# Kernel tuning notes

Hardware: AMD Instinct MI355X
Metric: run time of the kernel (lower is better)

The kernel has to match this reference:

```python
import jax, jax.numpy as jnp
import numpy as np

K = 3; STRIDE = 1; PAD = 1; DIL = 1; DG = 1  # deformable_groups = 1


def _conv2d(x, w, b, stride, pad):
    out = jax.lax.conv_general_dilated(
        x, w, (stride, stride), [(pad, pad), (pad, pad)],
        dimension_numbers=("NCHW", "OIHW", "NCHW"))
    return out + b[None, :, None, None]


def setup_inputs() -> dict:
    key = jax.random.key(0)
    k1, k2, k3 = jax.random.split(key, 3)
    B, Cin, H, W = 4, 64, 160, 160
    Cout = 64
    inp = {
        "input": jax.random.normal(k1, (B, Cin, H, W), dtype=jnp.float32),
        # offset/mask conv: dg*3*k*k = 27 output channels; scaled small so offsets are O(few px)
        "w_off": jax.random.normal(k2, (DG * 3 * K * K, Cin, K, K), dtype=jnp.float32) * 0.1,
        "b_off": jnp.zeros((DG * 3 * K * K,), dtype=jnp.float32),
        "w_dcn": jax.random.normal(k3, (Cout, Cin, K, K), dtype=jnp.float32) * 0.05,
        "b_dcn": jnp.zeros((Cout,), dtype=jnp.float32),
    }
    return inp


def _dcnv2(x, offset, mask, w, b):
    # x: [B,C,H,W]; offset: [B,2*kk,Ho,Wo]; mask: [B,kk,Ho,Wo] (already sigmoided)
    B, C, H, W = x.shape
    kk = K * K
    Ho, Wo = offset.shape[2], offset.shape[3]
    # mmcv channel layout within a deformable group: channel 2*p = y-offset, 2*p+1 = x-offset
    off = offset.reshape(B, kk, 2, Ho, Wo)
    off_y, off_x = off[:, :, 0], off[:, :, 1]            # [B,kk,Ho,Wo]

    ki, kj = jnp.meshgrid(jnp.arange(K), jnp.arange(K), indexing="ij")
    ki = ki.reshape(kk).astype(jnp.float32)
    kj = kj.reshape(kk).astype(jnp.float32)
    hs = (jnp.arange(Ho) * STRIDE - PAD).astype(jnp.float32)
    ws = (jnp.arange(Wo) * STRIDE - PAD).astype(jnp.float32)
    base_y = hs[None, :, None] + (ki * DIL)[:, None, None]   # [kk,Ho,1]
    base_x = ws[None, None, :] + (kj * DIL)[:, None, None]   # [kk,1,Wo]

    y = base_y[None] + off_y   # [B,kk,Ho,Wo]
    xx = base_x[None] + off_x

    y0 = jnp.floor(y); x0 = jnp.floor(xx)
    dy = y - y0; dx = xx - x0
    y0i = y0.astype(jnp.int32); y1i = y0i + 1
    x0i = x0.astype(jnp.int32); x1i = x0i + 1

    def gather(img, yi, xi):
        # img [C,H,W]; yi/xi [kk,Ho,Wo]; zero padding outside the image
        valid = (yi >= 0) & (yi < H) & (xi >= 0) & (xi < W)
        yc = jnp.clip(yi, 0, H - 1)
        xc = jnp.clip(xi, 0, W - 1)
        return img[:, yc, xc] * valid[None]   # [C,kk,Ho,Wo]

    gb = jax.vmap(gather)
    g00 = gb(x, y0i, x0i)
    g01 = gb(x, y0i, x1i)
    g10 = gb(x, y1i, x0i)
    g11 = gb(x, y1i, x1i)

    w00 = ((1 - dy) * (1 - dx))[:, None]   # [B,1,kk,Ho,Wo]
    w01 = ((1 - dy) * dx)[:, None]
    w10 = (dy * (1 - dx))[:, None]
    w11 = (dy * dx)[:, None]
    val = g00 * w00 + g01 * w01 + g10 * w10 + g11 * w11   # [B,C,kk,Ho,Wo]

    val = val * mask[:, None]                              # modulation
    Cout = w.shape[0]
    out = jnp.einsum("bckhw,ock->bohw", val, w.reshape(Cout, C, kk))
    return out + b[None, :, None, None]


def reference(input, w_off, b_off, w_dcn, b_dcn):
    om = _conv2d(input, w_off, b_off, STRIDE, PAD)   # [B, 3*kk, Ho, Wo]
    o1, o2, mask = jnp.split(om, 3, axis=1)
    offset = jnp.concatenate([o1, o2], axis=1)
    mask = jax.nn.sigmoid(mask)
    return _dcnv2(input, offset, mask, w_dcn, b_dcn)
```

## Files before the change

### kernel.cpp

```cpp
#include <hip/hip_runtime.h>
#include <math.h>

#define B_   4
#define CIN  64
#define H_   160
#define W_   160
#define COUT 64
#define OFFC 27
#define HW_  (H_ * W_)
#define NPIX (B_ * HW_)

#define TILE_P 64
#define VP2    65


__global__ __launch_bounds__(256) void k_transpose_nhwc(const float* __restrict__ in,
                                                        float* __restrict__ out) {
    __shared__ float tile[CIN][33];
    int blk = blockIdx.x;
    int wc  = blk % 5;
    int by  = blk / 5;
    int y   = by % H_;
    int b   = by / H_;
    int w0  = wc * 32;
    int t   = threadIdx.x;

    int wi = t & 31, ch = t >> 5;
#pragma unroll
    for (int r = 0; r < 8; ++r) {
        int c = r * 8 + ch;
        tile[c][wi] = in[((b * CIN + c) * H_ + y) * W_ + w0 + wi];
    }
    __syncthreads();
    int c2 = t & 63, wj = t >> 6;
#pragma unroll
    for (int r = 0; r < 8; ++r) {
        int wi2 = r * 4 + wj;
        out[((b * H_ + y) * W_ + w0 + wi2) * CIN + c2] = tile[c2][wi2];
    }
}

__global__ void k_transpose_w(const float* __restrict__ w, float* __restrict__ wT) {
    int i  = blockIdx.x * 256 + threadIdx.x;
    int co = i & 63;
    int kc = i >> 6;
    int c  = kc & 63;
    int k  = kc >> 6;
    wT[i] = w[(co * CIN + c) * 9 + k];
}

__global__ __launch_bounds__(256, 4) void k_offconv(const float* __restrict__ in,
                                                    const float* __restrict__ wo,
                                                    const float* __restrict__ bo,
                                                    float* __restrict__ om2) {
    int bid = (int)blockIdx.x;
    int id  = (bid & 7) * 150 + (bid >> 3);
    int g   = id % 3;
    int pb  = id / 3;
    int p   = pb * 256 + threadIdx.x;
    int b   = p / HW_;
    int rem = p - b * HW_;
    int y   = rem / W_;
    int x   = rem - y * W_;

    int   off[9];
    float valid[9];
#pragma unroll
    for (int di = 0; di < 3; ++di) {
        int yy = y + di - 1;
        int yc = min(max(yy, 0), H_ - 1);
        bool yok = (yy >= 0) & (yy < H_);
#pragma unroll
        for (int dj = 0; dj < 3; ++dj) {
            int xx = x + dj - 1;
            int xc = min(max(xx, 0), W_ - 1);
            bool ok = yok & (xx >= 0) & (xx < W_);
            off[di * 3 + dj]   = yc * W_ + xc;
            valid[di * 3 + dj] = ok ? 1.f : 0.f;
        }
    }

    float acc[9];
#pragma unroll
    for (int j = 0; j < 9; ++j) acc[j] = bo[g * 9 + j];

    const float* inb = in + (size_t)b * CIN * HW_;
    const float* wg  = wo + (size_t)(g * 9) * 576;
    for (int c = 0; c < CIN; c += 2) {
        float va[9], vb[9];
#pragma unroll
        for (int tp = 0; tp < 9; ++tp)
            va[tp] = inb[c * HW_ + off[tp]] * valid[tp];
#pragma unroll
        for (int tp = 0; tp < 9; ++tp)
            vb[tp] = inb[(c + 1) * HW_ + off[tp]] * valid[tp];
#pragma unroll
        for (int j = 0; j < 9; ++j) {
#pragma unroll
            for (int tp = 0; tp < 9; ++tp)
                acc[j] += va[tp] * wg[j * 576 + c * 9 + tp];
#pragma unroll
            for (int tp = 0; tp < 9; ++tp)
                acc[j] += vb[tp] * wg[j * 576 + (c + 1) * 9 + tp];
        }
    }
#pragma unroll
    for (int j = 0; j < 9; ++j)
        om2[(size_t)(g * 9 + j) * NPIX + p] = acc[j];
}

template <bool NHWC>
__global__ __launch_bounds__(256, 6) void k_dcn(const float* __restrict__ xsrc,
                                                const float* __restrict__ om2,
                                                const float* __restrict__ wT,
                                                const float* __restrict__ bd,
                                                float* __restrict__ out) {
    __shared__ __align__(16) float sk[TILE_P * 8];
    __shared__ __align__(16) float vals[64 * VP2];

    int t   = threadIdx.x;
    int bid = (int)blockIdx.x;
    int blk = (bid & 7) * ((NPIX / TILE_P) / 8) + (bid >> 3);
    int p0  = blk * TILE_P;
    int b   = p0 / HW_;
    int rb  = p0 - b * HW_;

    int lane = t & 63;
    int co0  = __builtin_amdgcn_readfirstlane((t >> 6) << 4);

    float acc[16];
#pragma unroll
    for (int j = 0; j < 16; ++j) acc[j] = bd[co0 + j];

    const float* base = xsrc + (size_t)b * CIN * HW_;

    for (int k = 0; k < 9; ++k) {
        __syncthreads();

        if (t < TILE_P) {
            int p   = p0 + t;
            int rem = rb + t;
            int y   = rem / W_;
            int x   = rem - y * W_;
            float oy = om2[(size_t)(2 * k) * NPIX + p];
            float ox = om2[(size_t)(2 * k + 1) * NPIX + p];
            float mr = om2[(size_t)(18 + k) * NPIX + p];
            float m  = 1.f / (1.f + expf(-mr));
            int ki = k / 3, kj = k - ki * 3;
            float fy  = (float)(y - 1 + ki) + oy;
            float fx  = (float)(x - 1 + kj) + ox;
            float fy0 = floorf(fy), fx0 = floorf(fx);
            float dy = fy - fy0, dx = fx - fx0;
            int iy = (int)fy0, ix = (int)fx0;
            bool yok0 = (iy >= 0) & (iy < H_);
            bool yok1 = (iy + 1 >= 0) & (iy + 1 < H_);
            bool xok0 = (ix >= 0) & (ix < W_);
            bool xok1 = (ix + 1 >= 0) & (ix + 1 < W_);
            int iyc0 = min(max(iy, 0), H_ - 1);
            int iyc1 = min(max(iy + 1, 0), H_ - 1);
            int ixc0 = min(max(ix, 0), W_ - 1);
            int ixc1 = min(max(ix + 1, 0), W_ - 1);
            const int mul = NHWC ? 64 : 1;
            float4 swt, sof;
            swt.x = (1.f - dy) * (1.f - dx) * m * (float)(yok0 & xok0);
            swt.y = (1.f - dy) * dx         * m * (float)(yok0 & xok1);
            swt.z = dy * (1.f - dx)         * m * (float)(yok1 & xok0);
            swt.w = dy * dx                 * m * (float)(yok1 & xok1);
            sof.x = __int_as_float((iyc0 * W_ + ixc0) * mul);
            sof.y = __int_as_float((iyc0 * W_ + ixc1) * mul);
            sof.z = __int_as_float((iyc1 * W_ + ixc0) * mul);
            sof.w = __int_as_float((iyc1 * W_ + ixc1) * mul);
            *reinterpret_cast<float4*>(sk + t * 8)     = swt;
            *reinterpret_cast<float4*>(sk + t * 8 + 4) = sof;
        }
        __syncthreads();

        {
            int c     = lane;
            int cterm = NHWC ? c : c * HW_;
#pragma unroll 4
            for (int it = 0; it < 16; ++it) {
                int pix = (t >> 6) + 4 * it;
                const float* s = sk + pix * 8;
                float4 sw = *reinterpret_cast<const float4*>(s);
                float4 so = *reinterpret_cast<const float4*>(s + 4);
                float g00 = base[__float_as_int(so.x) + cterm];
                float g01 = base[__float_as_int(so.y) + cterm];
                float g10 = base[__float_as_int(so.z) + cterm];
                float g11 = base[__float_as_int(so.w) + cterm];
                vals[c * VP2 + pix] = g00 * sw.x + g01 * sw.y + g10 * sw.z + g11 * sw.w;
            }
        }
        __syncthreads();

        const float* wk = wT + (k * 64) * 64 + co0;
#pragma unroll 4
        for (int c = 0; c < 64; ++c) {
            float v = vals[c * VP2 + lane];
            const float* wp = wk + c * 64;
            float4 wv0 = *reinterpret_cast<const float4*>(wp);
            float4 wv1 = *reinterpret_cast<const float4*>(wp + 4);
            float4 wv2 = *reinterpret_cast<const float4*>(wp + 8);
            float4 wv3 = *reinterpret_cast<const float4*>(wp + 12);
            acc[0]  += v * wv0.x;  acc[1]  += v * wv0.y;
            acc[2]  += v * wv0.z;  acc[3]  += v * wv0.w;
            acc[4]  += v * wv1.x;  acc[5]  += v * wv1.y;
            acc[6]  += v * wv1.z;  acc[7]  += v * wv1.w;
            acc[8]  += v * wv2.x;  acc[9]  += v * wv2.y;
            acc[10] += v * wv2.z;  acc[11] += v * wv2.w;
            acc[12] += v * wv3.x;  acc[13] += v * wv3.y;
            acc[14] += v * wv3.z;  acc[15] += v * wv3.w;
        }
    }

    __syncthreads();
#pragma unroll
    for (int j = 0; j < 16; ++j)
        vals[(co0 + j) * VP2 + lane] = acc[j];
    __syncthreads();
#pragma unroll 4
    for (int it = 0; it < 16; ++it) {
        int i  = t + it * 256;
        int co = i >> 6;
        int px = i & 63;
        out[((size_t)(b * COUT + co)) * HW_ + rb + px] = vals[co * VP2 + px];
    }
}

extern "C" void kernel_launch(void* const* d_in, const int* in_sizes, int n_in,
                              void* d_out, int out_size, void* d_ws, size_t ws_size,
                              hipStream_t stream) {
    const float* input = (const float*)d_in[0];
    const float* w_off = (const float*)d_in[1];
    const float* b_off = (const float*)d_in[2];
    const float* w_dcn = (const float*)d_in[3];
    const float* b_dcn = (const float*)d_in[4];
    float* out = (float*)d_out;

    const size_t XN_F = (size_t)NPIX * CIN;
    const size_t OM_F = (size_t)NPIX * OFFC;
    const size_t WT_F = 576 * 64;
    const size_t need_full = (XN_F + OM_F + WT_F) * sizeof(float);

    float* ws = (float*)d_ws;
    if (ws_size >= need_full) {
        float* x_nhwc = ws;
        float* om2    = ws + XN_F;
        float* wT     = om2 + OM_F;
        k_transpose_nhwc<<<dim3(B_ * H_ * 5), dim3(256), 0, stream>>>(input, x_nhwc);
        k_transpose_w<<<dim3(144), dim3(256), 0, stream>>>(w_dcn, wT);
        k_offconv<<<dim3(1200), dim3(256), 0, stream>>>(input, w_off, b_off, om2);
        k_dcn<true><<<dim3(NPIX / TILE_P), dim3(256), 0, stream>>>(x_nhwc, om2, wT, b_dcn, out);
    } else {
        float* om2 = ws;
        float* wT  = om2 + OM_F;
        k_transpose_w<<<dim3(144), dim3(256), 0, stream>>>(w_dcn, wT);
        k_offconv<<<dim3(1200), dim3(256), 0, stream>>>(input, w_off, b_off, om2);
        k_dcn<false><<<dim3(NPIX / TILE_P), dim3(256), 0, stream>>>(input, om2, wT, b_dcn, out);
    }
}
```

Before: 319.9 us.

## Precompute all tap sample weights and double-buffer gathered values in DCN kernel

The DCN kernel now computes bilinear weights and offsets for all 9 kernel taps up front using every thread, instead of 64 threads per tap. Gathered values are double-buffered in shared memory so the gather for tap k+1 overlaps the FMA accumulation for tap k, cutting the barriers per tap from three to one. This roughly doubles LDS use, so the occupancy hint drops from 6 to 3 blocks per CU. The offset conv loop is also changed from manual 2-channel unrolling to a pragma unroll 2.

```diff
diff --git a/kernel.cpp b/kernel.cpp
--- a/kernel.cpp
+++ b/kernel.cpp
@@ -86,22 +86,17 @@
 
     const float* inb = in + (size_t)b * CIN * HW_;
     const float* wg  = wo + (size_t)(g * 9) * 576;
-    for (int c = 0; c < CIN; c += 2) {
-        float va[9], vb[9];
+#pragma unroll 2
+    for (int c = 0; c < CIN; ++c) {
+        float v[9];
 #pragma unroll
         for (int tp = 0; tp < 9; ++tp)
-            va[tp] = inb[c * HW_ + off[tp]] * valid[tp];
-#pragma unroll
-        for (int tp = 0; tp < 9; ++tp)
-            vb[tp] = inb[(c + 1) * HW_ + off[tp]] * valid[tp];
+            v[tp] = inb[c * HW_ + off[tp]] * valid[tp];
 #pragma unroll
         for (int j = 0; j < 9; ++j) {
 #pragma unroll
             for (int tp = 0; tp < 9; ++tp)
-                acc[j] += va[tp] * wg[j * 576 + c * 9 + tp];
-#pragma unroll
-            for (int tp = 0; tp < 9; ++tp)
-                acc[j] += vb[tp] * wg[j * 576 + (c + 1) * 9 + tp];
+                acc[j] += v[tp] * wg[j * 576 + c * 9 + tp];
         }
     }
 #pragma unroll
@@ -110,13 +105,13 @@
 }
 
 template <bool NHWC>
-__global__ __launch_bounds__(256, 6) void k_dcn(const float* __restrict__ xsrc,
+__global__ __launch_bounds__(256, 3) void k_dcn(const float* __restrict__ xsrc,
                                                 const float* __restrict__ om2,
                                                 const float* __restrict__ wT,
                                                 const float* __restrict__ bd,
                                                 float* __restrict__ out) {
-    __shared__ __align__(16) float sk[TILE_P * 8];
-    __shared__ __align__(16) float vals[64 * VP2];
+    __shared__ __align__(16) float sk[9 * TILE_P * 8];
+    __shared__ __align__(16) float vals[2][64 * VP2];
 
     int t   = threadIdx.x;
     int bid = (int)blockIdx.x;
@@ -134,12 +129,14 @@
 
     const float* base = xsrc + (size_t)b * CIN * HW_;
 
-    for (int k = 0; k < 9; ++k) {
-        __syncthreads();
-
-        if (t < TILE_P) {
-            int p   = p0 + t;
-            int rem = rb + t;
+#pragma unroll
+    for (int it = 0; it < 3; ++it) {
+        int e = t + it * 256;
+        if (e < 9 * TILE_P) {
+            int k   = e >> 6;
+            int pix = e & 63;
+            int p   = p0 + pix;
+            int rem = rb + pix;
             int y   = rem / W_;
             int x   = rem - y * W_;
             float oy = om2[(size_t)(2 * k) * NPIX + p];
@@ -170,33 +167,53 @@
             sof.y = __int_as_float((iyc0 * W_ + ixc1) * mul);
             sof.z = __int_as_float((iyc1 * W_ + ixc0) * mul);
             sof.w = __int_as_float((iyc1 * W_ + ixc1) * mul);
-            *reinterpret_cast<float4*>(sk + t * 8)     = swt;
-            *reinterpret_cast<float4*>(sk + t * 8 + 4) = sof;
-        }
-        __syncthreads();
-
-        {
-            int c     = lane;
-            int cterm = NHWC ? c : c * HW_;
+            *reinterpret_cast<float4*>(sk + e * 8)     = swt;
+            *reinterpret_cast<float4*>(sk + e * 8 + 4) = sof;
+        }
+    }
+    __syncthreads();
+
+    int cterm = NHWC ? lane : lane * HW_;
+
+#pragma unroll 4
+    for (int it = 0; it < 16; ++it) {
+        int pix = (t >> 6) + 4 * it;
+        const float* s = sk + pix * 8;
+        float4 sw = *reinterpret_cast<const float4*>(s);
+        float4 so = *reinterpret_cast<const float4*>(s + 4);
+        float g00 = base[__float_as_int(so.x) + cterm];
+        float g01 = base[__float_as_int(so.y) + cterm];
+        float g10 = base[__float_as_int(so.z) + cterm];
+        float g11 = base[__float_as_int(so.w) + cterm];
+        vals[0][lane * VP2 + pix] = g00 * sw.x + g01 * sw.y + g10 * sw.z + g11 * sw.w;
+    }
+    __syncthreads();
+
+    for (int k = 0; k < 9; ++k) {
+        int cur = k & 1;
+
+        if (k < 8) {
+            const float* skt = sk + (k + 1) * TILE_P * 8;
+            float* vb = vals[cur ^ 1];
 #pragma unroll 4
             for (int it = 0; it < 16; ++it) {
                 int pix = (t >> 6) + 4 * it;
-                const float* s = sk + pix * 8;
+                const float* s = skt + pix * 8;
                 float4 sw = *reinterpret_cast<const float4*>(s);
                 float4 so = *reinterpret_cast<const float4*>(s + 4);
                 float g00 = base[__float_as_int(so.x) + cterm];
                 float g01 = base[__float_as_int(so.y) + cterm];
                 float g10 = base[__float_as_int(so.z) + cterm];
                 float g11 = base[__float_as_int(so.w) + cterm];
-                vals[c * VP2 + pix] = g00 * sw.x + g01 * sw.y + g10 * sw.z + g11 * sw.w;
+                vb[lane * VP2 + pix] = g00 * sw.x + g01 * sw.y + g10 * sw.z + g11 * sw.w;
             }
         }
-        __syncthreads();
-
+
+        const float* va = vals[cur];
         const float* wk = wT + (k * 64) * 64 + co0;
 #pragma unroll 4
         for (int c = 0; c < 64; ++c) {
-            float v = vals[c * VP2 + lane];
+            float v = va[c * VP2 + lane];
             const float* wp = wk + c * 64;
             float4 wv0 = *reinterpret_cast<const float4*>(wp);
             float4 wv1 = *reinterpret_cast<const float4*>(wp + 4);
@@ -211,19 +228,19 @@
             acc[12] += v * wv3.x;  acc[13] += v * wv3.y;
             acc[14] += v * wv3.z;  acc[15] += v * wv3.w;
         }
-    }
-
-    __syncthreads();
+        __syncthreads();
+    }
+
 #pragma unroll
     for (int j = 0; j < 16; ++j)
-        vals[(co0 + j) * VP2 + lane] = acc[j];
+        vals[0][(co0 + j) * VP2 + lane] = acc[j];
     __syncthreads();
 #pragma unroll 4
     for (int it = 0; it < 16; ++it) {
         int i  = t + it * 256;
         int co = i >> 6;
         int px = i & 63;
-        out[((size_t)(b * COUT + co)) * HW_ + rb + px] = vals[co * VP2 + px];
+        out[((size_t)(b * COUT + co)) * HW_ + rb + px] = vals[0][co * VP2 + px];
     }
 }
 
```

Result: no change. 324.2 us (+1.3%).
